# Kernel optimization log

Measured on AMD Instinct MI355X. Metric: run time of the kernel, lower is better.

Reference implementation:

```python
import jax, jax.numpy as jnp
import numpy as np

B, N = 256, 512          # trees, nodes per tree (topological order, root last)
IN, HID, OUT = 57, 512, 57  # len(ascii_letters + " .,;'") = 57


def setup_inputs() -> dict:
    rng = np.random.default_rng(0)
    # children indices strictly less than node index; -1 means absent child
    u = rng.random((B, N, 2))
    idx = np.arange(N)[None, :, None]
    ch = np.floor(u * (idx + 1)).astype(np.int32) - 1  # in [-1, i-1]
    left_idx = jnp.asarray(ch[..., 0])
    right_idx = jnp.asarray(ch[..., 1])
    values = jnp.asarray(rng.integers(0, IN, (B, N)), dtype=jnp.int32)
    key = jax.random.key(0)
    k1, k2, k3, k4 = jax.random.split(key, 4)
    s1 = 1.0 / np.sqrt(IN + HID)
    s2 = 1.0 / np.sqrt(HID)
    W_ih = jax.random.uniform(k1, (IN + HID, HID), minval=-s1, maxval=s1, dtype=jnp.float32)
    b_ih = jax.random.uniform(k2, (HID,), minval=-s1, maxval=s1, dtype=jnp.float32)
    W_o = jax.random.uniform(k3, (HID, OUT), minval=-s2, maxval=s2, dtype=jnp.float32)
    b_o = jax.random.uniform(k4, (OUT,), minval=-s2, maxval=s2, dtype=jnp.float32)
    return dict(left_idx=left_idx, right_idx=right_idx, values=values,
                W_ih=W_ih, b_ih=b_ih, W_o=W_o, b_o=b_o)


def _encode(left_idx, right_idx, values, W_ih, b_ih):
    # one-hot chars, precompute the input half of the concat+linear for all nodes
    X = jax.nn.one_hot(values, IN, dtype=W_ih.dtype)        # [B,N,IN]
    Wx, Wh = W_ih[:IN], W_ih[IN:]                            # split concat linear
    Xp = jnp.einsum('bni,ih->bnh', X, Wx) + b_ih             # [B,N,HID]
    SENT = N  # sentinel row holding zeros (hidden for None child)
    li = jnp.where(left_idx < 0, SENT, left_idx)             # [B,N]
    ri = jnp.where(right_idx < 0, SENT, right_idx)
    H0 = jnp.zeros((B, N + 1, HID), Xp.dtype)
    brange = jnp.arange(B)

    def step(H, inp):
        i, xp, l, r = inp                                    # xp:[B,HID], l/r:[B]
        hl = H[brange, l]                                    # gather child hiddens
        hr = H[brange, r]
        h = jnp.tanh(xp + (hl + hr) @ Wh)                    # recurrence
        H = H.at[:, i].set(h)
        return H, None

    xs = (jnp.arange(N), jnp.swapaxes(Xp, 0, 1), li.T, ri.T)
    H, _ = jax.lax.scan(step, H0, xs)
    return H[:, N - 1]                                       # root hidden [B,HID]


def reference(left_idx, right_idx, values, W_ih, b_ih, W_o, b_o):
    h_root = _encode(left_idx, right_idx, values, W_ih, b_ih)
    logits = h_root @ W_o + b_o                              # i2o
    return jax.nn.log_softmax(logits, axis=1)                # [B,OUT]
```

## Files before the change

kernel.cpp:

```cpp
#include <hip/hip_runtime.h>
#include <stdint.h>

#define BATCH 256
#define NNODE 512
#define INP   57
#define HIDD  512
#define OUTD  57

typedef int i32x4 __attribute__((ext_vector_type(4)));

__device__ __forceinline__ void gload_lds16(const void* g, void* l){
  __builtin_amdgcn_global_load_lds(
      (const __attribute__((address_space(1))) unsigned int*)g,
      (__attribute__((address_space(3))) unsigned int*)l, 16, 0, 0);
}

__global__ void pack_wq(const float* __restrict__ W_ih, const float* __restrict__ b_ih,
                        signed char* __restrict__ Wq){
  int idx = blockIdx.x * 256 + threadIdx.x;
  int j    =  idx        & 15;
  int lane = (idx >> 4)  & 63;
  int nt   = (idx >> 10) & 31;
  int kt   =  idx >> 15;
  int n    = nt * 16 + (lane & 15);
  int ksub = (lane >> 4) * 16 + j;
  const float scale = 127.0f * sqrtf((float)(INP + HIDD));
  float wv;
  if (kt < 8)            wv = W_ih[(size_t)(INP + kt * 64 + ksub) * HIDD + n];
  else if (ksub < INP)   wv = W_ih[(size_t)ksub * HIDD + n];
  else if (ksub == INP)  wv = b_ih[n];
  else                   wv = 0.0f;
  float q = rintf(wv * scale);
  q = fminf(127.0f, fmaxf(-127.0f, q));
  Wq[idx] = (signed char)q;
}

__device__ __forceinline__ void issue_gather(
    int m0, int Mcur, int w, int lane, int m16, int quad,
    signed char* __restrict__ Ab, signed char* __restrict__ Rb,
    const int* ord_s, const int* li_s, const int* ri_s, const int* val_s,
    signed char* Hb)
{
  const int kt   = w;
  const int koff = kt * 64 + quad * 16;
  #pragma unroll
  for (int mt = 0; mt < 2; ++mt) {
    const int row  = mt * 16 + m16;
    const int node = (row < Mcur) ? ord_s[m0 + row] : -1;
    const int loff = (node >= 0) ? li_s[node] : NNODE * HIDD;
    gload_lds16(Hb + (size_t)(loff + koff), Ab + (kt * 2 + mt) * 1024);
    const int roff = (node >= 0) ? ri_s[node] : NNODE * HIDD;
    gload_lds16(Hb + (size_t)(roff + koff), Rb + (kt * 2 + mt) * 1024);
  }
  if (w < 2) {
    const int erow  = w * 16 + m16;
    const int enode = (erow < Mcur) ? ord_s[m0 + erow] : -1;
    const int v     = (enode >= 0) ? val_s[enode] : -1;
    signed char bytes[16];
    #pragma unroll
    for (int j = 0; j < 16; ++j) {
      const int ks = quad * 16 + j;
      bytes[j] = (enode >= 0 && (ks == v || ks == INP)) ? (signed char)127 : (signed char)0;
    }
    *(i32x4*)(Ab + (16 + w) * 1024 + lane * 16) = *(const i32x4*)bytes;
  }
}

template<int NMT>
__device__ __forceinline__ void compute_chunk(
    int m0, int Mcur, int w, int lane, int m16, int quad,
    const signed char* __restrict__ Ab, const signed char* __restrict__ Rb,
    const int* ordoff_s, const i32x4 (&Bv)[9][4], signed char* Hb)
{
  i32x4 acc[NMT][4];
  #pragma unroll
  for (int mt = 0; mt < NMT; ++mt)
    #pragma unroll
    for (int nt = 0; nt < 4; ++nt)
      acc[mt][nt] = (i32x4){0, 0, 0, 0};

  #pragma unroll
  for (int kt = 0; kt < 8; ++kt) {
    #pragma unroll
    for (int mt = 0; mt < NMT; ++mt) {
      i32x4 al = *(const i32x4*)(Ab + (kt * 2 + mt) * 1024 + lane * 16);
      #pragma unroll
      for (int nt = 0; nt < 4; ++nt)
        acc[mt][nt] = __builtin_amdgcn_mfma_i32_16x16x64_i8(al, Bv[kt][nt], acc[mt][nt], 0, 0, 0);
      i32x4 ar = *(const i32x4*)(Rb + (kt * 2 + mt) * 1024 + lane * 16);
      #pragma unroll
      for (int nt = 0; nt < 4; ++nt)
        acc[mt][nt] = __builtin_amdgcn_mfma_i32_16x16x64_i8(ar, Bv[kt][nt], acc[mt][nt], 0, 0, 0);
    }
  }
  #pragma unroll
  for (int mt = 0; mt < NMT; ++mt) {
    i32x4 ax = *(const i32x4*)(Ab + (16 + mt) * 1024 + lane * 16);
    #pragma unroll
    for (int nt = 0; nt < 4; ++nt)
      acc[mt][nt] = __builtin_amdgcn_mfma_i32_16x16x64_i8(ax, Bv[8][nt], acc[mt][nt], 0, 0, 0);
  }

  const float SCLE = 2.8853900817779268f / (16129.0f * sqrtf((float)(INP + HIDD)));
  #pragma unroll
  for (int mt = 0; mt < NMT; ++mt) {
    #pragma unroll
    for (int rg = 0; rg < 4; ++rg) {
      const int rowc = mt * 16 + quad * 4 + rg;
      if (rowc < Mcur) {
        signed char* hp = Hb + (size_t)ordoff_s[m0 + rowc] + (w * 64 + m16);
        #pragma unroll
        for (int nt = 0; nt < 4; ++nt) {
          const float x  = (float)acc[mt][nt][rg] * SCLE;
          const float e  = __builtin_amdgcn_exp2f(x);
          const float r  = __builtin_amdgcn_rcpf(e + 1.0f);
          const float tq = fmaf(-254.0f, r, 127.0f);
          hp[nt * 16] = (signed char)__float2int_rn(tq);
        }
      }
    }
  }
}

__global__ __launch_bounds__(512, 2) void tree_rnn(
    const int* __restrict__ left, const int* __restrict__ right,
    const int* __restrict__ values,
    const float* __restrict__ W_ih, const float* __restrict__ b_ih,
    const float* __restrict__ W_o,  const float* __restrict__ b_o,
    const signed char* __restrict__ Wq,
    signed char* __restrict__ Hbuf, float* __restrict__ out)
{
  __shared__ __align__(16) signed char Abuf[2][18 * 1024];
  __shared__ __align__(16) signed char Rbuf[2][16 * 1024];
  __shared__ int li_s[NNODE], ri_s[NNODE], val_s[NNODE];
  __shared__ int lvl_s[NNODE], ord_s[NNODE], ordoff_s[NNODE];
  __shared__ int cnt_s[NNODE], cnt2_s[NNODE];
  __shared__ int offs_s[NNODE + 1];
  __shared__ int chg_s, lmax_s;
  __shared__ float hroot_s[HIDD];
  __shared__ float red_s[OUTD][8];
  __shared__ float logit_s[64];

  const int b    = blockIdx.x;
  const int tid  = threadIdx.x;
  const int lane = tid & 63;
  const int w    = tid >> 6;
  signed char* Hb = Hbuf + (size_t)b * (NNODE + 1) * HIDD;

  li_s[tid]  = left  [b * NNODE + tid];
  ri_s[tid]  = right [b * NNODE + tid];
  val_s[tid] = values[b * NNODE + tid];
  lvl_s[tid] = 0; cnt_s[tid] = 0; cnt2_s[tid] = 0;
  if (tid < 128) ((unsigned int*)(Hb + (size_t)NNODE * HIDD))[tid] = 0;
  if (tid == 0) lmax_s = 0;
  __syncthreads();

  for (;;) {
    if (tid == 0) chg_s = 0;
    __syncthreads();
    {
      int l = li_s[tid], r = ri_s[tid];
      int dl = (l >= 0) ? lvl_s[l] : -1;
      int dr = (r >= 0) ? lvl_s[r] : -1;
      int nl = 1 + (dl > dr ? dl : dr);
      if (nl > lvl_s[tid]) { lvl_s[tid] = nl; chg_s = 1; }
    }
    __syncthreads();
    if (!chg_s) break;
  }

  const int myl = lvl_s[tid];
  {
    int ml = myl;
    #pragma unroll
    for (int m = 1; m < 64; m <<= 1) ml = max(ml, __shfl_xor(ml, m, 64));
    if (lane == 0) atomicMax(&lmax_s, ml);
    atomicAdd(&cnt_s[myl], 1);
  }
  __syncthreads();
  const int Lmax = lmax_s;
  if (tid == 0) {
    int acc = 0;
    for (int L = 0; L <= Lmax; ++L) { offs_s[L] = acc; acc += cnt_s[L]; }
    offs_s[Lmax + 1] = acc;
  }
  __syncthreads();
  {
    int pos = offs_s[myl] + atomicAdd(&cnt2_s[myl], 1);
    ord_s[pos] = tid;
    ordoff_s[pos] = tid * HIDD;
  }
  __syncthreads();
  {
    int l = li_s[tid], r = ri_s[tid];
    li_s[tid] = (l < 0 ? NNODE : l) * HIDD;
    ri_s[tid] = (r < 0 ? NNODE : r) * HIDD;
  }

  const int m16  = lane & 15;
  const int quad = lane >> 4;

  i32x4 Bv[9][4];
  #pragma unroll
  for (int kt = 0; kt < 9; ++kt)
    #pragma unroll
    for (int nt = 0; nt < 4; ++nt)
      Bv[kt][nt] = *(const i32x4*)(Wq + ((size_t)(kt * 32 + 4 * w + nt) * 64 + lane) * 16);

  for (int L = 0; L <= Lmax; ++L) {
    const int start = offs_s[L], end = offs_s[L + 1];
    const int nch = (end - start + 31) >> 5;
    __syncthreads();
    issue_gather(start, min(32, end - start), w, lane, m16, quad,
                 Abuf[0], Rbuf[0], ord_s, li_s, ri_s, val_s, Hb);
    for (int c = 0; c < nch; ++c) {
      __syncthreads();
      const int m0 = start + c * 32;
      const int Mc = min(32, end - m0);
      if (c + 1 < nch) {
        const int m1 = m0 + 32;
        issue_gather(m1, min(32, end - m1), w, lane, m16, quad,
                     Abuf[(c + 1) & 1], Rbuf[(c + 1) & 1],
                     ord_s, li_s, ri_s, val_s, Hb);
      }
      const signed char* Ab = Abuf[c & 1];
      const signed char* Rb = Rbuf[c & 1];
      if (Mc > 16)
        compute_chunk<2>(m0, Mc, w, lane, m16, quad, Ab, Rb, ordoff_s, Bv, Hb);
      else
        compute_chunk<1>(m0, Mc, w, lane, m16, quad, Ab, Rb, ordoff_s, Bv, Hb);
    }
  }
  __syncthreads();

  hroot_s[tid] = (float)Hb[(size_t)(NNODE - 1) * HIDD + tid] * (1.0f / 127.0f);
  __syncthreads();
  {
    const int j = tid >> 3, part = tid & 7;
    if (j < OUTD) {
      float p = 0.f;
      const int k0 = part * 64;
      for (int k = k0; k < k0 + 64; ++k)
        p += hroot_s[k] * W_o[(size_t)k * OUTD + j];
      red_s[j][part] = p;
    }
  }
  __syncthreads();
  if (tid < OUTD) {
    float s = b_o[tid];
    #pragma unroll
    for (int p = 0; p < 8; ++p) s += red_s[tid][p];
    logit_s[tid] = s;
  }
  __syncthreads();
  if (w == 0) {
    float x = (lane < OUTD) ? logit_s[lane] : -1e30f;
    float mx = x;
    #pragma unroll
    for (int m = 1; m < 64; m <<= 1) mx = fmaxf(mx, __shfl_xor(mx, m, 64));
    float ex = (lane < OUTD) ? __expf(x - mx) : 0.f;
    float sm = ex;
    #pragma unroll
    for (int m = 1; m < 64; m <<= 1) sm += __shfl_xor(sm, m, 64);
    float ls = logf(sm);
    if (lane < OUTD) out[b * OUTD + lane] = x - mx - ls;
  }
}

extern "C" void kernel_launch(void* const* d_in, const int* in_sizes, int n_in,
                              void* d_out, int out_size, void* d_ws, size_t ws_size,
                              hipStream_t stream) {
  const int*   left   = (const int*)  d_in[0];
  const int*   right  = (const int*)  d_in[1];
  const int*   values = (const int*)  d_in[2];
  const float* W_ih   = (const float*)d_in[3];
  const float* b_ih   = (const float*)d_in[4];
  const float* W_o    = (const float*)d_in[5];
  const float* b_o    = (const float*)d_in[6];
  float* out = (float*)d_out;

  signed char* Wq   = (signed char*)d_ws;
  signed char* Hbuf = (signed char*)((char*)d_ws + 512 * 1024);

  pack_wq<<<1152, 256, 0, stream>>>(W_ih, b_ih, Wq);
  tree_rnn<<<BATCH, 512, 0, stream>>>(left, right, values, W_ih, b_ih, W_o, b_o,
                                      Wq, Hbuf, out);
}
```

Before: 209.9 us.

## Average child hiddens in int8 before MFMA to halve recurrent matmul work

Uses (hl+hr)@Wh = 2*avg(hl,hr)@Wh: the left and right child int8 hiddens are averaged bytewise in registers and one A operand is stored to LDS. This halves the recurrent MFMA count and removes the separate right-child LDS buffer. The input/bias weight tile is scaled by half and the tanh scale doubled to compensate. The async global-to-LDS loads become register prefetches written after compute. The rounding in the byte average adds quantization error, and the register staging can cost occupancy.

```diff
diff --git a/kernel.cpp b/kernel.cpp
--- a/kernel.cpp
+++ b/kernel.cpp
@@ -8,12 +8,6 @@
 #define OUTD  57
 
 typedef int i32x4 __attribute__((ext_vector_type(4)));
-
-__device__ __forceinline__ void gload_lds16(const void* g, void* l){
-  __builtin_amdgcn_global_load_lds(
-      (const __attribute__((address_space(1))) unsigned int*)g,
-      (__attribute__((address_space(3))) unsigned int*)l, 16, 0, 0);
-}
 
 __global__ void pack_wq(const float* __restrict__ W_ih, const float* __restrict__ b_ih,
                         signed char* __restrict__ Wq){
@@ -25,32 +19,62 @@
   int n    = nt * 16 + (lane & 15);
   int ksub = (lane >> 4) * 16 + j;
   const float scale = 127.0f * sqrtf((float)(INP + HIDD));
-  float wv;
+  float wv; float sc = scale;
   if (kt < 8)            wv = W_ih[(size_t)(INP + kt * 64 + ksub) * HIDD + n];
-  else if (ksub < INP)   wv = W_ih[(size_t)ksub * HIDD + n];
-  else if (ksub == INP)  wv = b_ih[n];
-  else                   wv = 0.0f;
-  float q = rintf(wv * scale);
+  else {
+    sc = scale * 0.5f;
+    if (ksub < INP)      wv = W_ih[(size_t)ksub * HIDD + n];
+    else if (ksub == INP) wv = b_ih[n];
+    else                 wv = 0.0f;
+  }
+  float q = rintf(wv * sc);
   q = fminf(127.0f, fmaxf(-127.0f, q));
   Wq[idx] = (signed char)q;
 }
 
-__device__ __forceinline__ void issue_gather(
-    int m0, int Mcur, int w, int lane, int m16, int quad,
-    signed char* __restrict__ Ab, signed char* __restrict__ Rb,
-    const int* ord_s, const int* li_s, const int* ri_s, const int* val_s,
-    signed char* Hb)
+__device__ __forceinline__ unsigned int avg_s8x4(unsigned int a, unsigned int b){
+#if __has_builtin(__builtin_amdgcn_lerp)
+  return __builtin_amdgcn_lerp(a ^ 0x80808080u, b ^ 0x80808080u, 0x01010101u) ^ 0x80808080u;
+#else
+  unsigned int au = a ^ 0x80808080u, bu = b ^ 0x80808080u;
+  unsigned int o = au | bu, x = au ^ bu;
+  return ((o - ((x >> 1) & 0x7F7F7F7Fu)) ^ 0x80808080u);
+#endif
+}
+
+struct Pref { uint4 l[2]; uint4 r[2]; };
+
+__device__ __forceinline__ Pref load_pref(
+    int m0, int Mcur, int w, int m16, int quad,
+    const int* ord_s, const int* li_s, const int* ri_s,
+    const signed char* Hb)
 {
-  const int kt   = w;
-  const int koff = kt * 64 + quad * 16;
+  Pref p;
+  const int koff = w * 64 + quad * 16;
   #pragma unroll
   for (int mt = 0; mt < 2; ++mt) {
     const int row  = mt * 16 + m16;
     const int node = (row < Mcur) ? ord_s[m0 + row] : -1;
     const int loff = (node >= 0) ? li_s[node] : NNODE * HIDD;
-    gload_lds16(Hb + (size_t)(loff + koff), Ab + (kt * 2 + mt) * 1024);
+    p.l[mt] = *(const uint4*)(Hb + (size_t)(loff + koff));
     const int roff = (node >= 0) ? ri_s[node] : NNODE * HIDD;
-    gload_lds16(Hb + (size_t)(roff + koff), Rb + (kt * 2 + mt) * 1024);
+    p.r[mt] = *(const uint4*)(Hb + (size_t)(roff + koff));
+  }
+  return p;
+}
+
+__device__ __forceinline__ void write_pref(
+    const Pref& p, int m0, int Mcur, int w, int lane, int m16, int quad,
+    signed char* __restrict__ Ab, const int* ord_s, const int* val_s)
+{
+  #pragma unroll
+  for (int mt = 0; mt < 2; ++mt) {
+    uint4 o;
+    o.x = avg_s8x4(p.l[mt].x, p.r[mt].x);
+    o.y = avg_s8x4(p.l[mt].y, p.r[mt].y);
+    o.z = avg_s8x4(p.l[mt].z, p.r[mt].z);
+    o.w = avg_s8x4(p.l[mt].w, p.r[mt].w);
+    *(uint4*)(Ab + (w * 2 + mt) * 1024 + lane * 16) = o;
   }
   if (w < 2) {
     const int erow  = w * 16 + m16;
@@ -69,7 +93,7 @@
 template<int NMT>
 __device__ __forceinline__ void compute_chunk(
     int m0, int Mcur, int w, int lane, int m16, int quad,
-    const signed char* __restrict__ Ab, const signed char* __restrict__ Rb,
+    const signed char* __restrict__ Ab,
     const int* ordoff_s, const i32x4 (&Bv)[9][4], signed char* Hb)
 {
   i32x4 acc[NMT][4];
@@ -83,14 +107,10 @@
   for (int kt = 0; kt < 8; ++kt) {
     #pragma unroll
     for (int mt = 0; mt < NMT; ++mt) {
-      i32x4 al = *(const i32x4*)(Ab + (kt * 2 + mt) * 1024 + lane * 16);
+      i32x4 a = *(const i32x4*)(Ab + (kt * 2 + mt) * 1024 + lane * 16);
       #pragma unroll
       for (int nt = 0; nt < 4; ++nt)
-        acc[mt][nt] = __builtin_amdgcn_mfma_i32_16x16x64_i8(al, Bv[kt][nt], acc[mt][nt], 0, 0, 0);
-      i32x4 ar = *(const i32x4*)(Rb + (kt * 2 + mt) * 1024 + lane * 16);
-      #pragma unroll
-      for (int nt = 0; nt < 4; ++nt)
-        acc[mt][nt] = __builtin_amdgcn_mfma_i32_16x16x64_i8(ar, Bv[kt][nt], acc[mt][nt], 0, 0, 0);
+        acc[mt][nt] = __builtin_amdgcn_mfma_i32_16x16x64_i8(a, Bv[kt][nt], acc[mt][nt], 0, 0, 0);
     }
   }
   #pragma unroll
@@ -101,7 +121,7 @@
       acc[mt][nt] = __builtin_amdgcn_mfma_i32_16x16x64_i8(ax, Bv[8][nt], acc[mt][nt], 0, 0, 0);
   }
 
-  const float SCLE = 2.8853900817779268f / (16129.0f * sqrtf((float)(INP + HIDD)));
+  const float SCLE = 5.7707801635558536f / (16129.0f * sqrtf((float)(INP + HIDD)));
   #pragma unroll
   for (int mt = 0; mt < NMT; ++mt) {
     #pragma unroll
@@ -131,7 +151,6 @@
     signed char* __restrict__ Hbuf, float* __restrict__ out)
 {
   __shared__ __align__(16) signed char Abuf[2][18 * 1024];
-  __shared__ __align__(16) signed char Rbuf[2][16 * 1024];
   __shared__ int li_s[NNODE], ri_s[NNODE], val_s[NNODE];
   __shared__ int lvl_s[NNODE], ord_s[NNODE], ordoff_s[NNODE];
   __shared__ int cnt_s[NNODE], cnt2_s[NNODE];
@@ -211,24 +230,29 @@
     const int start = offs_s[L], end = offs_s[L + 1];
     const int nch = (end - start + 31) >> 5;
     __syncthreads();
-    issue_gather(start, min(32, end - start), w, lane, m16, quad,
-                 Abuf[0], Rbuf[0], ord_s, li_s, ri_s, val_s, Hb);
+    {
+      Pref p0 = load_pref(start, min(32, end - start), w, m16, quad,
+                          ord_s, li_s, ri_s, Hb);
+      write_pref(p0, start, min(32, end - start), w, lane, m16, quad,
+                 Abuf[0], ord_s, val_s);
+    }
     for (int c = 0; c < nch; ++c) {
       __syncthreads();
       const int m0 = start + c * 32;
       const int Mc = min(32, end - m0);
-      if (c + 1 < nch) {
-        const int m1 = m0 + 32;
-        issue_gather(m1, min(32, end - m1), w, lane, m16, quad,
-                     Abuf[(c + 1) & 1], Rbuf[(c + 1) & 1],
-                     ord_s, li_s, ri_s, val_s, Hb);
-      }
+      Pref p;
+      const bool more = (c + 1 < nch);
+      if (more)
+        p = load_pref(m0 + 32, min(32, end - m0 - 32), w, m16, quad,
+                      ord_s, li_s, ri_s, Hb);
       const signed char* Ab = Abuf[c & 1];
-      const signed char* Rb = Rbuf[c & 1];
       if (Mc > 16)
-        compute_chunk<2>(m0, Mc, w, lane, m16, quad, Ab, Rb, ordoff_s, Bv, Hb);
+        compute_chunk<2>(m0, Mc, w, lane, m16, quad, Ab, ordoff_s, Bv, Hb);
       else
-        compute_chunk<1>(m0, Mc, w, lane, m16, quad, Ab, Rb, ordoff_s, Bv, Hb);
+        compute_chunk<1>(m0, Mc, w, lane, m16, quad, Ab, ordoff_s, Bv, Hb);
+      if (more)
+        write_pref(p, m0 + 32, min(32, end - m0 - 32), w, lane, m16, quad,
+                   Abuf[(c + 1) & 1], ord_s, val_s);
     }
   }
   __syncthreads();
```

Result: no change. 212.5 us (+1.2%).
